# Optimization experiments

Hardware: AMD Instinct MI355X
Metric: run time of the kernel (lower is better)

Reference implementation:

```python
import jax, jax.numpy as jnp
import numpy as np

EMBED_DIM = 512
NUM_HEADS = 16
HEAD_DIM = EMBED_DIM // NUM_HEADS
SCALING = (HEAD_DIM * 1.0) ** (-0.5)
N_NODE, N_GRAPH = 1024, 4


def setup_inputs() -> dict:
    key = jax.random.key(0)
    ks = jax.random.split(key, 6)
    lim_in = 1.0 / np.sqrt(EMBED_DIM)
    query = jax.random.normal(ks[0], (N_NODE, N_GRAPH, EMBED_DIM), dtype=jnp.float32)
    attn_bias = jax.random.normal(ks[1], (N_GRAPH * NUM_HEADS, N_NODE, N_NODE), dtype=jnp.float32)
    # torch nn.Linear stores weight as [out_features, in_features]
    W_in = jax.random.uniform(ks[2], (3 * EMBED_DIM, EMBED_DIM), jnp.float32, -lim_in, lim_in)
    b_in = jax.random.uniform(ks[3], (3 * EMBED_DIM,), jnp.float32, -lim_in, lim_in)
    W_out = jax.random.uniform(ks[4], (EMBED_DIM, EMBED_DIM), jnp.float32, -lim_in, lim_in)
    b_out = jax.random.uniform(ks[5], (EMBED_DIM,), jnp.float32, -lim_in, lim_in)
    return {"query": query, "attn_bias": attn_bias, "W_in": W_in, "b_in": b_in,
            "W_out": W_out, "b_out": b_out}


def reference(query, attn_bias, W_in, b_in, W_out, b_out):
    n_node, n_graph, embed_dim = query.shape
    H, D = NUM_HEADS, HEAD_DIM
    # in_proj then chunk into q, k, v along last dim
    qkv = query @ W_in.T + b_in                       # [N, G, 3E]
    q, k, v = jnp.split(qkv, 3, axis=-1)              # each [N, G, E]
    q = q.reshape(n_node, n_graph, H, D) * SCALING
    k = k.reshape(n_node, n_graph, H, D)
    v = v.reshape(n_node, n_graph, H, D)
    # scores: [G, H, N, N] -> flatten to [G*H, N, N] to add bias
    scores = jnp.einsum('nghd,mghd->ghnm', q, k).reshape(n_graph * H, n_node, n_node)
    scores = scores + attn_bias
    probs = jax.nn.softmax(scores, axis=-1)           # dropout=0.0 / eval: no-op
    probs = probs.reshape(n_graph, H, n_node, n_node)
    attn = jnp.einsum('ghnm,mghd->nghd', probs, v).reshape(n_node, n_graph, embed_dim)
    return attn @ W_out.T + b_out
```

## Files before the change

kernel.cpp:

```cpp
#include <hip/hip_runtime.h>
#include <hip/hip_bf16.h>
#include <stdint.h>
#include <stddef.h>

typedef __attribute__((ext_vector_type(8))) short bfrag8;
typedef __attribute__((ext_vector_type(4))) float facc4;

#define SCALING 0.17677669529663687f

__device__ __forceinline__ unsigned short f2bf(float f) {
  union { float f; unsigned u; } v; v.f = f;
  unsigned r = v.u + 0x7fffu + ((v.u >> 16) & 1u);
  return (unsigned short)(r >> 16);
}

__global__ __launch_bounds__(256)
void convert_bf16(const float* __restrict__ q, const float* __restrict__ wi,
                  const float* __restrict__ wo,
                  unsigned short* __restrict__ qb, unsigned short* __restrict__ wib,
                  unsigned short* __restrict__ wob) {
  int t = blockIdx.x * 256 + threadIdx.x;
  const float4* src; unsigned short* dst; int idx;
  if (t < 524288)            { src = (const float4*)q;  dst = qb;  idx = t; }
  else if (t < 524288+196608){ src = (const float4*)wi; dst = wib; idx = t - 524288; }
  else                       { src = (const float4*)wo; dst = wob; idx = t - 720896; }
  float4 v = src[idx];
  ushort4 o;
  o.x = f2bf(v.x); o.y = f2bf(v.y); o.z = f2bf(v.z); o.w = f2bf(v.w);
  *(ushort4*)(dst + (size_t)idx * 4) = o;
}

template<int MODE>
__global__ __launch_bounds__(256, 2)
void gemm_bt(const unsigned short* __restrict__ A, const unsigned short* __restrict__ Bw,
             const float* __restrict__ bias,
             unsigned short* __restrict__ oQ, unsigned short* __restrict__ oK,
             unsigned short* __restrict__ oV, float* __restrict__ oF) {
  constexpr int K = 512;
  __shared__ __align__(16) unsigned short lA[2][64 * 32];
  __shared__ __align__(16) unsigned short lB[2][128 * 32];
  const int t = threadIdx.x;
  const int w = t >> 6, l = t & 63;
  const int lr = l & 15, lg = l >> 4;
  const int mBase = blockIdx.x * 64;
  const int nBase = blockIdx.y * 128;
  const int wr = w >> 1, wc = w & 1;

  facc4 acc[2][4];
#pragma unroll
  for (int i = 0; i < 2; i++)
#pragma unroll
    for (int j = 0; j < 4; j++) acc[i][j] = (facc4){0.f, 0.f, 0.f, 0.f};

  const int arow = t & 63, aslot = t >> 6;
  const unsigned short* aSrc = A + (size_t)(mBase + arow) * K + aslot * 8;
  const int bcol0 = t & 127, bslot0 = t >> 7;
  const int bcol1 = (256 + t) & 127, bslot1 = (256 + t) >> 7;
  const unsigned short* bSrc0 = Bw + (size_t)(nBase + bcol0) * K + bslot0 * 8;
  const unsigned short* bSrc1 = Bw + (size_t)(nBase + bcol1) * K + bslot1 * 8;

  auto stage = [&](int ks, int buf) {
    const int kB = ks * 32;
    *(int4*)(&lA[buf][(size_t)t * 8])         = *(const int4*)(aSrc + kB);
    *(int4*)(&lB[buf][(size_t)t * 8])         = *(const int4*)(bSrc0 + kB);
    *(int4*)(&lB[buf][(size_t)(256 + t) * 8]) = *(const int4*)(bSrc1 + kB);
  };

  stage(0, 0);
  __syncthreads();
#pragma unroll 1
  for (int ks = 0; ks < 16; ks++) {
    const int buf = ks & 1;
    if (ks < 15) stage(ks + 1, buf ^ 1);
    bfrag8 af[2], bfr[4];
#pragma unroll
    for (int qi = 0; qi < 2; qi++)
      af[qi] = *(const bfrag8*)(&lA[buf][(lg * 64 + wr * 32 + qi * 16 + lr) * 8]);
#pragma unroll
    for (int nj = 0; nj < 4; nj++)
      bfr[nj] = *(const bfrag8*)(&lB[buf][(lg * 128 + wc * 64 + nj * 16 + lr) * 8]);
#pragma unroll
    for (int qi = 0; qi < 2; qi++)
#pragma unroll
      for (int nj = 0; nj < 4; nj++)
        acc[qi][nj] = __builtin_amdgcn_mfma_f32_16x16x32_bf16(af[qi], bfr[nj], acc[qi][nj], 0, 0, 0);
    __syncthreads();
  }

#pragma unroll
  for (int qi = 0; qi < 2; qi++)
#pragma unroll
    for (int nj = 0; nj < 4; nj++) {
      int m0 = mBase + wr * 32 + qi * 16 + lg * 4;
      int o = nBase + wc * 64 + nj * 16 + lr;
      float bv = bias[o];
#pragma unroll
      for (int r = 0; r < 4; r++) {
        float v = acc[qi][nj][r] + bv;
        int mm = m0 + r;
        if (MODE == 0) {
          int n = mm >> 2, g = mm & 3;
          int chunk = o >> 9, cc = o & 511, h = cc >> 5, d = cc & 31;
          size_t oidx = ((size_t)(g * 16 + h) * 1024 + n) * 32 + d;
          if (chunk == 0)      oQ[oidx] = f2bf(v * SCALING);
          else if (chunk == 1) oK[oidx] = f2bf(v);
          else                 oV[oidx] = f2bf(v);
        } else {
          oF[(size_t)mm * 512 + o] = v;
        }
      }
    }
}

__global__ __launch_bounds__(256)
void transpose_v(const unsigned short* __restrict__ V, unsigned short* __restrict__ Vt) {
  __shared__ unsigned short tile[32][264];
  const int gh = blockIdx.x, n0 = blockIdx.y * 256;
  const int t = threadIdx.x;
  const unsigned short* src = V + ((size_t)gh * 1024 + n0) * 32;
#pragma unroll
  for (int c = 0; c < 4; c++) {
    int j = c * 256 + t; int row = j >> 2, d0 = (j & 3) * 8;
    bfrag8 v = *(const bfrag8*)(src + (size_t)row * 32 + d0);
#pragma unroll
    for (int i = 0; i < 8; i++) tile[d0 + i][row] = (unsigned short)v[i];
  }
  __syncthreads();
  unsigned short* dst = Vt + (size_t)gh * 32 * 1024 + n0;
#pragma unroll
  for (int c = 0; c < 4; c++) {
    int j = c * 256 + t; int d = j >> 5, n8 = (j & 31) * 8;
    *(bfrag8*)(dst + (size_t)d * 1024 + n8) = *(const bfrag8*)(&tile[d][n8]);
  }
}

__global__ __launch_bounds__(256)
void attn_kernel(const unsigned short* __restrict__ Qs, const unsigned short* __restrict__ Ks,
                 const unsigned short* __restrict__ Vt, const float* __restrict__ biasG,
                 unsigned short* __restrict__ Out) {
  __shared__ __align__(16) unsigned short Pl[4][16 * 64];
  const int gh = blockIdx.x, q0 = blockIdx.y * 64;
  const int t = threadIdx.x, w = t >> 6, l = t & 63;
  const int lr = l & 15, lg = l >> 4;

  const unsigned short* Qg = Qs + (size_t)gh * 1024 * 32;
  const unsigned short* Kg = Ks + (size_t)gh * 1024 * 32;
  const unsigned short* Vg = Vt + (size_t)gh * 32 * 1024;
  const float* Bt = biasG + (size_t)gh * 1048576 + (size_t)(q0 + w * 16 + lg * 4) * 1024 + lr;

  bfrag8 qf = *(const bfrag8*)(Qg + (size_t)(q0 + w * 16 + lr) * 32 + lg * 8);

  facc4 accO[2];
  accO[0] = (facc4){0.f, 0.f, 0.f, 0.f};
  accO[1] = (facc4){0.f, 0.f, 0.f, 0.f};
  float mrun[4], lrun[4];
#pragma unroll
  for (int r = 0; r < 4; r++) { mrun[r] = -3.0e38f; lrun[r] = 0.f; }

  unsigned short* Pw = Pl[w];

#pragma unroll 1
  for (int kt = 0; kt < 16; kt++) {
    const int kb = kt * 64;
    facc4 sc[4];
#pragma unroll
    for (int j = 0; j < 4; j++)
#pragma unroll
      for (int r = 0; r < 4; r++)
        sc[j][r] = Bt[(size_t)r * 1024 + kb + j * 16];
#pragma unroll
    for (int j = 0; j < 4; j++) {
      bfrag8 kf = *(const bfrag8*)(Kg + (size_t)(kb + j * 16 + lr) * 32 + lg * 8);
      sc[j] = __builtin_amdgcn_mfma_f32_16x16x32_bf16(qf, kf, sc[j], 0, 0, 0);
    }
    float tm[4];
#pragma unroll
    for (int r = 0; r < 4; r++) tm[r] = -3.0e38f;
#pragma unroll
    for (int j = 0; j < 4; j++)
#pragma unroll
      for (int r = 0; r < 4; r++) tm[r] = fmaxf(tm[r], sc[j][r]);
#pragma unroll
    for (int mk = 1; mk < 16; mk <<= 1)
#pragma unroll
      for (int r = 0; r < 4; r++) tm[r] = fmaxf(tm[r], __shfl_xor(tm[r], mk, 64));
    float scale[4];
#pragma unroll
    for (int r = 0; r < 4; r++) {
      float mn = fmaxf(mrun[r], tm[r]);
      scale[r] = __expf(mrun[r] - mn);
      mrun[r] = mn;
    }
    float rs[4] = {0.f, 0.f, 0.f, 0.f};
#pragma unroll
    for (int j = 0; j < 4; j++)
#pragma unroll
      for (int r = 0; r < 4; r++) {
        float p = __expf(sc[j][r] - mrun[r]);
        rs[r] += p;
        int row = lg * 4 + r, col = j * 16 + lr;
        int byte = (row * 128 + col * 2) ^ ((row & 7) << 4);
        *(unsigned short*)((char*)Pw + byte) = f2bf(p);
      }
#pragma unroll
    for (int mk = 1; mk < 16; mk <<= 1)
#pragma unroll
      for (int r = 0; r < 4; r++) rs[r] += __shfl_xor(rs[r], mk, 64);
#pragma unroll
    for (int r = 0; r < 4; r++) lrun[r] = lrun[r] * scale[r] + rs[r];
#pragma unroll
    for (int h = 0; h < 2; h++)
#pragma unroll
      for (int r = 0; r < 4; r++) accO[h][r] *= scale[r];
#pragma unroll
    for (int ksb = 0; ksb < 2; ksb++) {
      int byte = (lr * 128 + (ksb * 32 + lg * 8) * 2) ^ ((lr & 7) << 4);
      bfrag8 pf = *(const bfrag8*)((char*)Pw + byte);
#pragma unroll
      for (int h = 0; h < 2; h++) {
        bfrag8 vf = *(const bfrag8*)(Vg + (size_t)(h * 16 + lr) * 1024 + kb + ksb * 32 + lg * 8);
        accO[h] = __builtin_amdgcn_mfma_f32_16x16x32_bf16(pf, vf, accO[h], 0, 0, 0);
      }
    }
  }

  const int g = gh >> 4, hh = gh & 15;
#pragma unroll
  for (int h = 0; h < 2; h++)
#pragma unroll
    for (int r = 0; r < 4; r++) {
      int q = q0 + w * 16 + lg * 4 + r;
      float v = accO[h][r] / lrun[r];
      int e = hh * 32 + h * 16 + lr;
      Out[(size_t)(q * 4 + g) * 512 + e] = f2bf(v);
    }
}

extern "C" void kernel_launch(void* const* d_in, const int* in_sizes, int n_in,
                              void* d_out, int out_size, void* d_ws, size_t ws_size,
                              hipStream_t stream) {
  (void)in_sizes; (void)n_in; (void)out_size; (void)ws_size;
  const float* query = (const float*)d_in[0];
  const float* abias = (const float*)d_in[1];
  const float* W_in  = (const float*)d_in[2];
  const float* b_in  = (const float*)d_in[3];
  const float* W_out = (const float*)d_in[4];
  const float* b_out = (const float*)d_in[5];
  float* out = (float*)d_out;
  char* ws = (char*)d_ws;
  unsigned short* qbf  = (unsigned short*)(ws);
  unsigned short* wibf = (unsigned short*)(ws + 4194304);
  unsigned short* wobf = (unsigned short*)(ws + 5767168);
  unsigned short* Qs   = (unsigned short*)(ws + 6291456);
  unsigned short* Ks   = (unsigned short*)(ws + 10485760);
  unsigned short* Vv   = (unsigned short*)(ws + 14680064);
  unsigned short* Vt   = (unsigned short*)(ws + 18874368);
  unsigned short* attO = (unsigned short*)(ws + 23068672);

  convert_bf16<<<3072, 256, 0, stream>>>(query, W_in, W_out, qbf, wibf, wobf);
  gemm_bt<0><<<dim3(64, 12), 256, 0, stream>>>(qbf, wibf, b_in, Qs, Ks, Vv, nullptr);
  transpose_v<<<dim3(64, 4), 256, 0, stream>>>(Vv, Vt);
  attn_kernel<<<dim3(64, 16), 256, 0, stream>>>(Qs, Ks, Vt, abias, attO);
  gemm_bt<1><<<dim3(64, 4), 256, 0, stream>>>(attO, wobf, b_out, nullptr, nullptr, nullptr, out);
}
```

Measured before the change: 122.5 us.

## Split attention over key halves with combine kernel; write V transposed from GEMM

The attention kernel now splits the key range into two halves along a third grid dimension. Each half writes unnormalized partial outputs plus running max and sum, and a new combine kernel merges them with a log-sum-exp rescale. This doubles the block count from 1024 to 2048, which should give better occupancy across the CUs. The QKV GEMM epilogue now writes V directly in transposed layout, so the separate transpose kernel is removed. The costs are extra fp32 partial-output traffic, one added launch, and strided scalar stores for V in the GEMM epilogue.

Measured after the change: 138.8 us. +13.3%, slower.

```diff
diff --git a/kernel.cpp b/kernel.cpp
--- a/kernel.cpp
+++ b/kernel.cpp
@@ -101,10 +101,12 @@
         if (MODE == 0) {
           int n = mm >> 2, g = mm & 3;
           int chunk = o >> 9, cc = o & 511, h = cc >> 5, d = cc & 31;
-          size_t oidx = ((size_t)(g * 16 + h) * 1024 + n) * 32 + d;
-          if (chunk == 0)      oQ[oidx] = f2bf(v * SCALING);
-          else if (chunk == 1) oK[oidx] = f2bf(v);
-          else                 oV[oidx] = f2bf(v);
+          if (chunk == 0)
+            oQ[((size_t)(g * 16 + h) * 1024 + n) * 32 + d] = f2bf(v * SCALING);
+          else if (chunk == 1)
+            oK[((size_t)(g * 16 + h) * 1024 + n) * 32 + d] = f2bf(v);
+          else
+            oV[((size_t)(g * 16 + h) * 32 + d) * 1024 + n] = f2bf(v);
         } else {
           oF[(size_t)mm * 512 + o] = v;
         }
@@ -113,33 +115,11 @@
 }
 
 __global__ __launch_bounds__(256)
-void transpose_v(const unsigned short* __restrict__ V, unsigned short* __restrict__ Vt) {
-  __shared__ unsigned short tile[32][264];
-  const int gh = blockIdx.x, n0 = blockIdx.y * 256;
-  const int t = threadIdx.x;
-  const unsigned short* src = V + ((size_t)gh * 1024 + n0) * 32;
-#pragma unroll
-  for (int c = 0; c < 4; c++) {
-    int j = c * 256 + t; int row = j >> 2, d0 = (j & 3) * 8;
-    bfrag8 v = *(const bfrag8*)(src + (size_t)row * 32 + d0);
-#pragma unroll
-    for (int i = 0; i < 8; i++) tile[d0 + i][row] = (unsigned short)v[i];
-  }
-  __syncthreads();
-  unsigned short* dst = Vt + (size_t)gh * 32 * 1024 + n0;
-#pragma unroll
-  for (int c = 0; c < 4; c++) {
-    int j = c * 256 + t; int d = j >> 5, n8 = (j & 31) * 8;
-    *(bfrag8*)(dst + (size_t)d * 1024 + n8) = *(const bfrag8*)(&tile[d][n8]);
-  }
-}
-
-__global__ __launch_bounds__(256)
 void attn_kernel(const unsigned short* __restrict__ Qs, const unsigned short* __restrict__ Ks,
                  const unsigned short* __restrict__ Vt, const float* __restrict__ biasG,
-                 unsigned short* __restrict__ Out) {
+                 float* __restrict__ Op, float* __restrict__ Ml) {
   __shared__ __align__(16) unsigned short Pl[4][16 * 64];
-  const int gh = blockIdx.x, q0 = blockIdx.y * 64;
+  const int gh = blockIdx.x, q0 = blockIdx.y * 64, z = blockIdx.z;
   const int t = threadIdx.x, w = t >> 6, l = t & 63;
   const int lr = l & 15, lg = l >> 4;
 
@@ -160,7 +140,7 @@
   unsigned short* Pw = Pl[w];
 
 #pragma unroll 1
-  for (int kt = 0; kt < 16; kt++) {
+  for (int kt = z * 8; kt < z * 8 + 8; kt++) {
     const int kb = kt * 64;
     facc4 sc[4];
 #pragma unroll
@@ -224,16 +204,41 @@
     }
   }
 
-  const int g = gh >> 4, hh = gh & 15;
+  const size_t pb = (size_t)(z * 64 + gh) * 1024;
 #pragma unroll
   for (int h = 0; h < 2; h++)
 #pragma unroll
     for (int r = 0; r < 4; r++) {
       int q = q0 + w * 16 + lg * 4 + r;
-      float v = accO[h][r] / lrun[r];
-      int e = hh * 32 + h * 16 + lr;
-      Out[(size_t)(q * 4 + g) * 512 + e] = f2bf(v);
-    }
+      Op[(pb + q) * 32 + h * 16 + lr] = accO[h][r];
+    }
+  if (lr == 0) {
+#pragma unroll
+    for (int r = 0; r < 4; r++) {
+      int q = q0 + w * 16 + lg * 4 + r;
+      Ml[(pb + q) * 2]     = mrun[r];
+      Ml[(pb + q) * 2 + 1] = lrun[r];
+    }
+  }
+}
+
+__global__ __launch_bounds__(256)
+void combine_kernel(const float* __restrict__ Op, const float* __restrict__ Ml,
+                    unsigned short* __restrict__ Out) {
+  int idx = blockIdx.x * 256 + threadIdx.x;
+  int d = idx & 31;
+  int n = (idx >> 5) & 1023;
+  int gh = idx >> 15;
+  size_t p0 = (size_t)gh * 1024 + n;
+  size_t p1 = (size_t)(64 + gh) * 1024 + n;
+  float m0 = Ml[p0 * 2], l0 = Ml[p0 * 2 + 1];
+  float m1 = Ml[p1 * 2], l1 = Ml[p1 * 2 + 1];
+  float m = fmaxf(m0, m1);
+  float a0 = __expf(m0 - m), a1 = __expf(m1 - m);
+  float linv = 1.0f / (l0 * a0 + l1 * a1);
+  float o = (Op[p0 * 32 + d] * a0 + Op[p1 * 32 + d] * a1) * linv;
+  int g = gh >> 4, hh = gh & 15;
+  Out[((size_t)(n * 4 + g)) * 512 + hh * 32 + d] = f2bf(o);
 }
 
 extern "C" void kernel_launch(void* const* d_in, const int* in_sizes, int n_in,
@@ -253,13 +258,14 @@
   unsigned short* wobf = (unsigned short*)(ws + 5767168);
   unsigned short* Qs   = (unsigned short*)(ws + 6291456);
   unsigned short* Ks   = (unsigned short*)(ws + 10485760);
-  unsigned short* Vv   = (unsigned short*)(ws + 14680064);
-  unsigned short* Vt   = (unsigned short*)(ws + 18874368);
-  unsigned short* attO = (unsigned short*)(ws + 23068672);
+  unsigned short* Vt   = (unsigned short*)(ws + 14680064);
+  unsigned short* attO = (unsigned short*)(ws + 18874368);
+  float*          Op   = (float*)(ws + 23068672);
+  float*          Ml   = (float*)(ws + 39845888);
 
   convert_bf16<<<3072, 256, 0, stream>>>(query, W_in, W_out, qbf, wibf, wobf);
-  gemm_bt<0><<<dim3(64, 12), 256, 0, stream>>>(qbf, wibf, b_in, Qs, Ks, Vv, nullptr);
-  transpose_v<<<dim3(64, 4), 256, 0, stream>>>(Vv, Vt);
-  attn_kernel<<<dim3(64, 16), 256, 0, stream>>>(Qs, Ks, Vt, abias, attO);
+  gemm_bt<0><<<dim3(64, 12), 256, 0, stream>>>(qbf, wibf, b_in, Qs, Ks, Vt, nullptr);
+  attn_kernel<<<dim3(64, 16, 2), 256, 0, stream>>>(Qs, Ks, Vt, abias, Op, Ml);
+  combine_kernel<<<8192, 256, 0, stream>>>(Op, Ml, attO);
   gemm_bt<1><<<dim3(64, 4), 256, 0, stream>>>(attO, wobf, b_out, nullptr, nullptr, nullptr, out);
 }
```

## Transpose QK^T MFMA so each lane owns one query row for vectorized bias loads

Applied to the files above, without the earlier changes.

Swaps the MFMA operand order so the score accumulator is transposed and each lane holds four consecutive key columns of a single query row. The attention bias can then be read with one float4 load per tile instead of four strided scalar loads, and the per-row max and sum reductions drop from four rows times four shuffles to a single value with two shuffles. Probabilities are packed into 64-bit LDS stores, while the rescale factors and final normalizers are redistributed to the P·V accumulator layout with extra shuffles. This relies on the new LDS byte addressing matching the transposed layout.

After: 128.8 us. 5.1% more time.

```diff
diff --git a/kernel.cpp b/kernel.cpp
--- a/kernel.cpp
+++ b/kernel.cpp
@@ -146,16 +146,14 @@
   const unsigned short* Qg = Qs + (size_t)gh * 1024 * 32;
   const unsigned short* Kg = Ks + (size_t)gh * 1024 * 32;
   const unsigned short* Vg = Vt + (size_t)gh * 32 * 1024;
-  const float* Bt = biasG + (size_t)gh * 1048576 + (size_t)(q0 + w * 16 + lg * 4) * 1024 + lr;
+  const float* Bq = biasG + (size_t)gh * 1048576 + (size_t)(q0 + w * 16 + lr) * 1024;
 
   bfrag8 qf = *(const bfrag8*)(Qg + (size_t)(q0 + w * 16 + lr) * 32 + lg * 8);
 
   facc4 accO[2];
   accO[0] = (facc4){0.f, 0.f, 0.f, 0.f};
   accO[1] = (facc4){0.f, 0.f, 0.f, 0.f};
-  float mrun[4], lrun[4];
-#pragma unroll
-  for (int r = 0; r < 4; r++) { mrun[r] = -3.0e38f; lrun[r] = 0.f; }
+  float mrun = -3.0e38f, lrun = 0.f;
 
   unsigned short* Pw = Pl[w];
 
@@ -165,56 +163,52 @@
     facc4 sc[4];
 #pragma unroll
     for (int j = 0; j < 4; j++)
-#pragma unroll
-      for (int r = 0; r < 4; r++)
-        sc[j][r] = Bt[(size_t)r * 1024 + kb + j * 16];
+      sc[j] = *(const facc4*)(Bq + kb + j * 16 + lg * 4);
 #pragma unroll
     for (int j = 0; j < 4; j++) {
       bfrag8 kf = *(const bfrag8*)(Kg + (size_t)(kb + j * 16 + lr) * 32 + lg * 8);
-      sc[j] = __builtin_amdgcn_mfma_f32_16x16x32_bf16(qf, kf, sc[j], 0, 0, 0);
-    }
-    float tm[4];
-#pragma unroll
-    for (int r = 0; r < 4; r++) tm[r] = -3.0e38f;
+      sc[j] = __builtin_amdgcn_mfma_f32_16x16x32_bf16(kf, qf, sc[j], 0, 0, 0);
+    }
+    float tm = sc[0][0];
 #pragma unroll
     for (int j = 0; j < 4; j++)
 #pragma unroll
-      for (int r = 0; r < 4; r++) tm[r] = fmaxf(tm[r], sc[j][r]);
-#pragma unroll
-    for (int mk = 1; mk < 16; mk <<= 1)
-#pragma unroll
-      for (int r = 0; r < 4; r++) tm[r] = fmaxf(tm[r], __shfl_xor(tm[r], mk, 64));
-    float scale[4];
-#pragma unroll
-    for (int r = 0; r < 4; r++) {
-      float mn = fmaxf(mrun[r], tm[r]);
-      scale[r] = __expf(mrun[r] - mn);
-      mrun[r] = mn;
-    }
-    float rs[4] = {0.f, 0.f, 0.f, 0.f};
-#pragma unroll
-    for (int j = 0; j < 4; j++)
-#pragma unroll
-      for (int r = 0; r < 4; r++) {
-        float p = __expf(sc[j][r] - mrun[r]);
-        rs[r] += p;
-        int row = lg * 4 + r, col = j * 16 + lr;
-        int byte = (row * 128 + col * 2) ^ ((row & 7) << 4);
-        *(unsigned short*)((char*)Pw + byte) = f2bf(p);
-      }
-#pragma unroll
-    for (int mk = 1; mk < 16; mk <<= 1)
-#pragma unroll
-      for (int r = 0; r < 4; r++) rs[r] += __shfl_xor(rs[r], mk, 64);
-#pragma unroll
-    for (int r = 0; r < 4; r++) lrun[r] = lrun[r] * scale[r] + rs[r];
+      for (int r = 0; r < 4; r++) tm = fmaxf(tm, sc[j][r]);
+    tm = fmaxf(tm, __shfl_xor(tm, 16, 64));
+    tm = fmaxf(tm, __shfl_xor(tm, 32, 64));
+    float mn = fmaxf(mrun, tm);
+    float scale = __expf(mrun - mn);
+    mrun = mn;
+    float rs = 0.f;
+    uint2 pk[4];
+#pragma unroll
+    for (int j = 0; j < 4; j++) {
+      float p0 = __expf(sc[j][0] - mn);
+      float p1 = __expf(sc[j][1] - mn);
+      float p2 = __expf(sc[j][2] - mn);
+      float p3 = __expf(sc[j][3] - mn);
+      rs += (p0 + p1) + (p2 + p3);
+      pk[j].x = (unsigned)f2bf(p0) | ((unsigned)f2bf(p1) << 16);
+      pk[j].y = (unsigned)f2bf(p2) | ((unsigned)f2bf(p3) << 16);
+    }
+    rs += __shfl_xor(rs, 16, 64);
+    rs += __shfl_xor(rs, 32, 64);
+    lrun = lrun * scale + rs;
+#pragma unroll
+    for (int j = 0; j < 4; j++) {
+      int byte = (lr * 128 + j * 32 + lg * 8) ^ ((lr & 7) << 4);
+      *(uint2*)((char*)Pw + byte) = pk[j];
+    }
+    float sc_pv[4];
+#pragma unroll
+    for (int r = 0; r < 4; r++) sc_pv[r] = __shfl(scale, lg * 4 + r, 64);
 #pragma unroll
     for (int h = 0; h < 2; h++)
 #pragma unroll
-      for (int r = 0; r < 4; r++) accO[h][r] *= scale[r];
+      for (int r = 0; r < 4; r++) accO[h][r] *= sc_pv[r];
 #pragma unroll
     for (int ksb = 0; ksb < 2; ksb++) {
-      int byte = (lr * 128 + (ksb * 32 + lg * 8) * 2) ^ ((lr & 7) << 4);
+      int byte = (lr * 128 + ksb * 64 + lg * 16) ^ ((lr & 7) << 4);
       bfrag8 pf = *(const bfrag8*)((char*)Pw + byte);
 #pragma unroll
       for (int h = 0; h < 2; h++) {
@@ -224,13 +218,16 @@
     }
   }
 
+  float lr_pv[4];
+#pragma unroll
+  for (int r = 0; r < 4; r++) lr_pv[r] = __shfl(lrun, lg * 4 + r, 64);
   const int g = gh >> 4, hh = gh & 15;
 #pragma unroll
   for (int h = 0; h < 2; h++)
 #pragma unroll
     for (int r = 0; r < 4; r++) {
       int q = q0 + w * 16 + lg * 4 + r;
-      float v = accO[h][r] / lrun[r];
+      float v = accO[h][r] / lr_pv[r];
       int e = hh * 32 + h * 16 + lr;
       Out[(size_t)(q * 4 + g) * 512 + e] = f2bf(v);
     }
```

## Double-buffer attention bias tiles into LDS via async global_load_lds

Applied to the files above, without the earlier changes.

The per-thread strided global loads of the fp32 attention bias are replaced by asynchronous global-to-LDS copies (global_load_lds) into a double-buffered, XOR-swizzled shared tile covering 128 keys per stage. Each stage of the loop computes two 64-key sub-blocks while the next bias tile is in flight, with explicit vmcnt waits and sched barriers controlling the overlap. The goal is to hide the latency of the dominant bias stream and make its loads coalesced. In exchange it adds 64 KB of LDS per block, which lowers occupancy, and depends on hand-tuned vmcnt counts that also count the K/V global loads.

After: 135.4 us. 10.6% more time.

```diff
diff --git a/kernel.cpp b/kernel.cpp
--- a/kernel.cpp
+++ b/kernel.cpp
@@ -138,15 +138,20 @@
 void attn_kernel(const unsigned short* __restrict__ Qs, const unsigned short* __restrict__ Ks,
                  const unsigned short* __restrict__ Vt, const float* __restrict__ biasG,
                  unsigned short* __restrict__ Out) {
+  __shared__ __align__(16) float biasT[2][64][128];
   __shared__ __align__(16) unsigned short Pl[4][16 * 64];
   const int gh = blockIdx.x, q0 = blockIdx.y * 64;
   const int t = threadIdx.x, w = t >> 6, l = t & 63;
   const int lr = l & 15, lg = l >> 4;
 
-  const unsigned short* Qg = Qs + (size_t)gh * 1024 * 32;
-  const unsigned short* Kg = Ks + (size_t)gh * 1024 * 32;
-  const unsigned short* Vg = Vt + (size_t)gh * 32 * 1024;
-  const float* Bt = biasG + (size_t)gh * 1048576 + (size_t)(q0 + w * 16 + lg * 4) * 1024 + lr;
+  const unsigned short* Qg = Qs + (size_t)gh * 32768;
+  const unsigned short* Kg = Ks + (size_t)gh * 32768;
+  const unsigned short* Vg = Vt + (size_t)gh * 32768;
+  const float* Bw = biasG + (size_t)gh * 1048576 + (size_t)(q0 + w * 16) * 1024;
+
+  const int rpair  = l >> 5;
+  const int chunkB = ((l >> 2) & 7) << 6;
+  const int subB   = (l & 3) << 4;
 
   bfrag8 qf = *(const bfrag8*)(Qg + (size_t)(q0 + w * 16 + lr) * 32 + lg * 8);
 
@@ -159,69 +164,98 @@
 
   unsigned short* Pw = Pl[w];
 
+  auto stageBias = [&](int bt, int buf) {
+#pragma unroll
+    for (int i = 0; i < 8; i++) {
+      const int key = ((i >> 1) & 3) << 6;
+      const char* src = (const char*)(Bw + (size_t)(i * 2 + rpair) * 1024 + bt * 128)
+                        + ((chunkB ^ key) + subB);
+      __builtin_amdgcn_global_load_lds(
+          (const __attribute__((address_space(1))) unsigned int*)src,
+          (__attribute__((address_space(3))) unsigned int*)(&biasT[buf][w * 16 + i * 2][0]),
+          16, 0, 0);
+    }
+  };
+
+  stageBias(0, 0);
+  stageBias(1, 1);
+
 #pragma unroll 1
-  for (int kt = 0; kt < 16; kt++) {
-    const int kb = kt * 64;
-    facc4 sc[4];
-#pragma unroll
-    for (int j = 0; j < 4; j++)
-#pragma unroll
-      for (int r = 0; r < 4; r++)
-        sc[j][r] = Bt[(size_t)r * 1024 + kb + j * 16];
-#pragma unroll
-    for (int j = 0; j < 4; j++) {
-      bfrag8 kf = *(const bfrag8*)(Kg + (size_t)(kb + j * 16 + lr) * 32 + lg * 8);
-      sc[j] = __builtin_amdgcn_mfma_f32_16x16x32_bf16(qf, kf, sc[j], 0, 0, 0);
-    }
-    float tm[4];
-#pragma unroll
-    for (int r = 0; r < 4; r++) tm[r] = -3.0e38f;
-#pragma unroll
-    for (int j = 0; j < 4; j++)
-#pragma unroll
-      for (int r = 0; r < 4; r++) tm[r] = fmaxf(tm[r], sc[j][r]);
-#pragma unroll
-    for (int mk = 1; mk < 16; mk <<= 1)
-#pragma unroll
-      for (int r = 0; r < 4; r++) tm[r] = fmaxf(tm[r], __shfl_xor(tm[r], mk, 64));
-    float scale[4];
-#pragma unroll
-    for (int r = 0; r < 4; r++) {
-      float mn = fmaxf(mrun[r], tm[r]);
-      scale[r] = __expf(mrun[r] - mn);
-      mrun[r] = mn;
-    }
-    float rs[4] = {0.f, 0.f, 0.f, 0.f};
-#pragma unroll
-    for (int j = 0; j < 4; j++)
+  for (int bt = 0; bt < 8; bt++) {
+    const int buf = bt & 1;
+    if (bt == 7) asm volatile("s_waitcnt vmcnt(0)" ::: "memory");
+    else         asm volatile("s_waitcnt vmcnt(8)" ::: "memory");
+    __builtin_amdgcn_sched_barrier(0);
+
+#pragma unroll
+    for (int s64 = 0; s64 < 2; s64++) {
+      const int kb = bt * 128 + s64 * 64;
+      facc4 sc[4];
+#pragma unroll
+      for (int j = 0; j < 4; j++)
+#pragma unroll
+        for (int r = 0; r < 4; r++)
+          sc[j][r] = *(const float*)((const char*)&biasT[buf][w * 16 + lg * 4 + r][0]
+                       + ((((s64 * 4 + j) ^ lg) << 6) + (lr << 2)));
+#pragma unroll
+      for (int j = 0; j < 4; j++) {
+        bfrag8 kf = *(const bfrag8*)(Kg + (size_t)(kb + j * 16 + lr) * 32 + lg * 8);
+        sc[j] = __builtin_amdgcn_mfma_f32_16x16x32_bf16(qf, kf, sc[j], 0, 0, 0);
+      }
+      float tm[4];
+#pragma unroll
+      for (int r = 0; r < 4; r++) tm[r] = -3.0e38f;
+#pragma unroll
+      for (int j = 0; j < 4; j++)
+#pragma unroll
+        for (int r = 0; r < 4; r++) tm[r] = fmaxf(tm[r], sc[j][r]);
+#pragma unroll
+      for (int mk = 1; mk < 16; mk <<= 1)
+#pragma unroll
+        for (int r = 0; r < 4; r++) tm[r] = fmaxf(tm[r], __shfl_xor(tm[r], mk, 64));
+      float scale[4];
 #pragma unroll
       for (int r = 0; r < 4; r++) {
-        float p = __expf(sc[j][r] - mrun[r]);
-        rs[r] += p;
-        int row = lg * 4 + r, col = j * 16 + lr;
-        int byte = (row * 128 + col * 2) ^ ((row & 7) << 4);
-        *(unsigned short*)((char*)Pw + byte) = f2bf(p);
-      }
-#pragma unroll
-    for (int mk = 1; mk < 16; mk <<= 1)
-#pragma unroll
-      for (int r = 0; r < 4; r++) rs[r] += __shfl_xor(rs[r], mk, 64);
-#pragma unroll
-    for (int r = 0; r < 4; r++) lrun[r] = lrun[r] * scale[r] + rs[r];
-#pragma unroll
-    for (int h = 0; h < 2; h++)
-#pragma unroll
-      for (int r = 0; r < 4; r++) accO[h][r] *= scale[r];
-#pragma unroll
-    for (int ksb = 0; ksb < 2; ksb++) {
-      int byte = (lr * 128 + (ksb * 32 + lg * 8) * 2) ^ ((lr & 7) << 4);
-      bfrag8 pf = *(const bfrag8*)((char*)Pw + byte);
-#pragma unroll
-      for (int h = 0; h < 2; h++) {
-        bfrag8 vf = *(const bfrag8*)(Vg + (size_t)(h * 16 + lr) * 1024 + kb + ksb * 32 + lg * 8);
-        accO[h] = __builtin_amdgcn_mfma_f32_16x16x32_bf16(pf, vf, accO[h], 0, 0, 0);
-      }
-    }
+        float mn = fmaxf(mrun[r], tm[r]);
+        scale[r] = __expf(mrun[r] - mn);
+        mrun[r] = mn;
+      }
+      float rs[4] = {0.f, 0.f, 0.f, 0.f};
+#pragma unroll
+      for (int j = 0; j < 4; j++)
+#pragma unroll
+        for (int r = 0; r < 4; r++) {
+          float p = __expf(sc[j][r] - mrun[r]);
+          rs[r] += p;
+          int row = lg * 4 + r, col = j * 16 + lr;
+          int byte = (row * 128 + col * 2) ^ ((row & 7) << 4);
+          *(unsigned short*)((char*)Pw + byte) = f2bf(p);
+        }
+#pragma unroll
+      for (int mk = 1; mk < 16; mk <<= 1)
+#pragma unroll
+        for (int r = 0; r < 4; r++) rs[r] += __shfl_xor(rs[r], mk, 64);
+#pragma unroll
+      for (int r = 0; r < 4; r++) lrun[r] = lrun[r] * scale[r] + rs[r];
+#pragma unroll
+      for (int h = 0; h < 2; h++)
+#pragma unroll
+        for (int r = 0; r < 4; r++) accO[h][r] *= scale[r];
+#pragma unroll
+      for (int ksb = 0; ksb < 2; ksb++) {
+        int byte = (lr * 128 + (ksb * 32 + lg * 8) * 2) ^ ((lr & 7) << 4);
+        bfrag8 pf = *(const bfrag8*)((char*)Pw + byte);
+#pragma unroll
+        for (int h = 0; h < 2; h++) {
+          bfrag8 vf = *(const bfrag8*)(Vg + (size_t)(h * 16 + lr) * 1024 + kb + ksb * 32 + lg * 8);
+          accO[h] = __builtin_amdgcn_mfma_f32_16x16x32_bf16(pf, vf, accO[h], 0, 0, 0);
+        }
+      }
+    }
+
+    __builtin_amdgcn_sched_barrier(0);
+    if (bt < 6) stageBias(bt + 2, buf);
+    __builtin_amdgcn_sched_barrier(0);
   }
 
   const int g = gh >> 4, hh = gh & 15;
```
